# Performance work log

Hardware: AMD Instinct MI355X
Metric: run time of the kernel (lower is better)

The kernel has to match this reference:

```python
import jax, jax.numpy as jnp
import numpy as np
import math

B, L, D_MODEL, D_K, H = 2, 1024, 1024, 1024, 16
HD = D_K // H  # 64, even
EPS = 1e-5


def setup_inputs() -> dict:
    key = jax.random.key(0)
    ks = jax.random.split(key, 16)
    s = 0.02
    inp = {
        'word_embed': jax.random.normal(ks[0], (B, L, D_MODEL), jnp.float32),
        'speaker_embed': jax.random.normal(ks[1], (B, L, D_MODEL), jnp.float32),
        'mask': jnp.broadcast_to(jnp.tril(jnp.ones((L, L), jnp.int32)), (B, L, L)),
        'qw_w': jax.random.normal(ks[2], (D_K, D_MODEL), jnp.float32) * s,
        'qw_b': jnp.zeros((D_K,), jnp.float32),
        'kw_w': jax.random.normal(ks[3], (D_K, D_MODEL), jnp.float32) * s,
        'kw_b': jnp.zeros((D_K,), jnp.float32),
        'qs_w': jax.random.normal(ks[4], (D_K, D_MODEL), jnp.float32) * s,
        'qs_b': jnp.zeros((D_K,), jnp.float32),
        'ks_w': jax.random.normal(ks[5], (D_K, D_MODEL), jnp.float32) * s,
        'ks_b': jnp.zeros((D_K,), jnp.float32),
        'v_w': jax.random.normal(ks[6], (D_K, D_MODEL), jnp.float32) * s,
        'v_b': jnp.zeros((D_K,), jnp.float32),
        'out_w': jax.random.normal(ks[7], (D_MODEL, D_K), jnp.float32) * s,
        'out_b': jnp.zeros((D_MODEL,), jnp.float32),
        'gamma': jnp.ones((HD,), jnp.float32),
        'beta': jnp.zeros((HD,), jnp.float32),
    }
    return inp


def _rotary_tables(seq_len, dim, dtype):
    pos = jnp.arange(seq_len, dtype=dtype)[:, None]  # [L,1]
    div = jnp.exp(jnp.arange(0, dim, 2, dtype=dtype) * (-math.log(10000.0) / dim))
    return jnp.sin(pos * div), jnp.cos(pos * div)  # each [L, dim//2]


def _rotary(x, sin, cos):
    # x: [B,H,L,HD]; NOTE: original concatenates halves (non-interleaved output)
    x1, x2 = x[..., 0::2], x[..., 1::2]
    return jnp.concatenate([x1 * cos - x2 * sin, x1 * sin + x2 * cos], axis=-1)


def _layernorm(x, gamma, beta):
    mu = jnp.mean(x, axis=-1, keepdims=True)
    var = jnp.mean(jnp.square(x - mu), axis=-1, keepdims=True)
    return (x - mu) * jax.lax.rsqrt(var + EPS) * gamma + beta


def _split(x):
    b, l, _ = x.shape
    return x.reshape(b, l, H, HD).transpose(0, 2, 1, 3)  # [B,H,L,HD]


def reference(word_embed, speaker_embed, mask, qw_w, qw_b, kw_w, kw_b,
              qs_w, qs_b, ks_w, ks_b, v_w, v_b, out_w, out_b, gamma, beta):
    proj = lambda x, w, b: jnp.einsum('bld,kd->blk', x, w) + b
    qw = _split(proj(word_embed, qw_w, qw_b))
    kw = _split(proj(word_embed, kw_w, kw_b))
    qs = _split(proj(speaker_embed, qs_w, qs_b))
    ks = _split(proj(speaker_embed, ks_w, ks_b))
    v = _split(proj(word_embed, v_w, v_b))

    sin, cos = _rotary_tables(word_embed.shape[1], HD, word_embed.dtype)
    ln = lambda x: _layernorm(_rotary(x, sin, cos), gamma, beta)
    qw, kw, qs, ks = ln(qw), ln(kw), ln(qs), ln(ks)

    scores = (jnp.einsum('bhqd,bhkd->bhqk', qw, kw)
              + jnp.einsum('bhqd,bhkd->bhqk', qs, ks)) / math.sqrt(2 * HD)
    scores = jnp.where(mask[:, None] == 0, -jnp.inf, scores)
    attn = jax.nn.softmax(scores, axis=-1)  # dropout is eval-mode no-op
    out = jnp.einsum('bhqk,bhkd->bhqd', attn, v)
    out = out.transpose(0, 2, 1, 3).reshape(out.shape[0], out.shape[2], D_K)
    out = jnp.einsum('blk,dk->bld', out, out_w) + out_b
    return (out, attn)
```

## Files before the change

### kernel.cpp

```cpp
#include <hip/hip_runtime.h>
#include <cstdint>
#include <cstddef>

typedef __bf16 bf16x8 __attribute__((ext_vector_type(8)));
typedef float  f32x4  __attribute__((ext_vector_type(4)));
typedef unsigned short ushort8_t __attribute__((ext_vector_type(8)));

__device__ __forceinline__ unsigned short f2bf(float f){
  unsigned u = __builtin_bit_cast(unsigned, f);
  u += 0x7fffu + ((u >> 16) & 1u);
  return (unsigned short)(u >> 16);
}
__device__ __forceinline__ float bf2f(unsigned short s){
  return __builtin_bit_cast(float, ((unsigned)s) << 16);
}

#define MFMA16(a,b,c) __builtin_amdgcn_mfma_f32_16x16x32_bf16((a),(b),(c),0,0,0)

__device__ __forceinline__ void gload16(const void* g, void* lds){
  __builtin_amdgcn_global_load_lds(
      (const __attribute__((address_space(1))) void*)g,
      (__attribute__((address_space(3))) void*)lds, 16, 0, 0);
}

// ... 25 lines not shown
    float ang = (float)pos * inv;
    float sv, cv; sincosf(ang, &sv, &cv);
    FB[5120 + idx]         = sv;
    FB[5120 + 32768 + idx] = cv;
  } else if (idx < 33792){
    int i = idx - 32768;
    FB[i] = qwb[i]; FB[1024+i] = kwb[i]; FB[2048+i] = vb[i];
    FB[3072+i] = qsb[i]; FB[3072+1024+i] = ksb[i];
  }

  const size_t total = 2621440;
  for (size_t c = (size_t)blockIdx.x*256 + threadIdx.x; c < total;
       c += (size_t)gridDim.x*256){
    const float* src; size_t dst; size_t i;
    if (c < 524288)       { src = word; dst = E_XW; i = c; }
    else if (c < 1048576) { src = spk;  dst = E_XS; i = c - 524288; }
    else {
      size_t t = c - 1048576; int seg = (int)(t >> 18); i = t & 262143;
      switch (seg){
        case 0:  src = qww; dst = E_WWORD;                      break;
        case 1:  src = kww; dst = E_WWORD + (size_t)1048576;    break;
        case 2:  src = vw;  dst = E_WWORD + (size_t)2097152;    break;
        case 3:  src = qsw; dst = E_WSPK;                       break;
        case 4:  src = ksw; dst = E_WSPK  + (size_t)1048576;    break;
        default: src = outw; dst = E_WOUT;                      break;
      }
    }
    float4 v = ((const float4*)src)[i];
    ushort4 o; o.x = f2bf(v.x); o.y = f2bf(v.y); o.z = f2bf(v.z); o.w = f2bf(v.w);
    ((ushort4*)(wsb + dst))[i] = o;
  }
}

template<int NF>
__device__ __forceinline__ void gemm_body(
    const unsigned short* __restrict__ A, const unsigned short* __restrict__ Bw,
    const float* __restrict__ bias, void* __restrict__ Cv,
    int N, int K, int bid, int out_bf16,
    unsigned short* As, unsigned short* Bs)
{
  const int BN = NF*32;
  const int nbn = N / BN;
  const int bm = bid / nbn, bn = bid % nbn;
  const int tid = threadIdx.x;
  const int l = tid & 63, w = tid >> 6;
  const int wm = w >> 1, wn = w & 1;
  const int li = l & 15, lg = l >> 4;

  f32x4 acc[4][NF];
  #pragma unroll
  for (int a = 0; a < 4; a++)
    #pragma unroll
    for (int b = 0; b < NF; b++) acc[a][b] = (f32x4){0.f,0.f,0.f,0.f};

  const int colS = (l & 3) * 8;
  const size_t aBase = (size_t)(bm*128) * K;
  const size_t bBase = (size_t)(bn*BN) * K;

  for (int kt = 0; kt < K; kt += 32){
    #pragma unroll
    for (int j = 0; j < 2; j++){
      int row = (w*2 + j)*16 + (l >> 2);
      gload16(A + aBase + (size_t)row*K + kt + colS, &As[(size_t)(w*2+j)*512]);
    }
    if (NF == 4){
      #pragma unroll
      for (int j = 0; j < 2; j++){
        int row = (w*2 + j)*16 + (l >> 2);
        gload16(Bw + bBase + (size_t)row*K + kt + colS, &Bs[(size_t)(w*2+j)*512]);
      }
    } else {
      int row = w*16 + (l >> 2);
      gload16(Bw + bBase + (size_t)row*K + kt + colS, &Bs[(size_t)w*512]);
    }
    asm volatile("s_waitcnt vmcnt(0)" ::: "memory");
    __syncthreads();

    bf16x8 af[4], bfr[NF];
    const int ko = lg * 8;
    #pragma unroll
    for (int fm = 0; fm < 4; fm++)
      af[fm] = *(const bf16x8*)&As[(wm*64 + fm*16 + li)*32 + ko];
    #pragma unroll
    for (int fn = 0; fn < NF; fn++)
      bfr[fn] = *(const bf16x8*)&Bs[(wn*(NF*16) + fn*16 + li)*32 + ko];
    #pragma unroll
    for (int fm = 0; fm < 4; fm++)
      #pragma unroll
      for (int fn = 0; fn < NF; fn++)
        acc[fm][fn] = MFMA16(af[fm], bfr[fn], acc[fm][fn]);
    __syncthreads();
  }

  #pragma unroll
  for (int fm = 0; fm < 4; fm++){
    int m0 = bm*128 + wm*64 + fm*16 + lg*4;
    #pragma unroll
    for (int fn = 0; fn < NF; fn++){
      int n = bn*BN + wn*(NF*16) + fn*16 + li;
      float bv = bias ? bias[n] : 0.f;
      #pragma unroll
      for (int r = 0; r < 4; r++){
        float v = acc[fm][fn][r] + bv;
        if (out_bf16) ((unsigned short*)Cv)[(size_t)(m0+r)*N + n] = f2bf(v);
        else          ((float*)Cv)[(size_t)(m0+r)*N + n] = v;
      }
    }
  }
}

__global__ __launch_bounds__(256) void gemm_qkv(
    const unsigned short* __restrict__ XW, const unsigned short* __restrict__ WWORD,
    const unsigned short* __restrict__ XS, const unsigned short* __restrict__ WSPK,
    const float* __restrict__ FB,
    unsigned short* __restrict__ PWORD, unsigned short* __restrict__ PSPK)
{
  __shared__ unsigned short As[128*32];
  __shared__ unsigned short Bs[128*32];
  int bid = blockIdx.x;
  if (bid < 384)
    gemm_body<4>(XW, WWORD, FB,        PWORD, 3072, 1024, bid,       1, As, Bs);
  else
    gemm_body<4>(XS, WSPK,  FB + 3072, PSPK,  2048, 1024, bid - 384, 1, As, Bs);
}

__global__ __launch_bounds__(256) void gemm_out(
    const unsigned short* __restrict__ CTX, const unsigned short* __restrict__ WOUT,
    const float* __restrict__ outb, float* __restrict__ outp)
{
  __shared__ unsigned short As[128*32];
  __shared__ unsigned short Bs[64*32];
  gemm_body<2>(CTX, WOUT, outb, outp, 1024, 1024, blockIdx.x, 0, As, Bs);
}

__global__ __launch_bounds__(256) void postproc(
    unsigned short* __restrict__ Pw, unsigned short* __restrict__ Ps,
    const float* __restrict__ gamma, const float* __restrict__ beta,
    const float* __restrict__ TS, const float* __restrict__ TC,
    unsigned short* __restrict__ VT)
{
  __shared__ float lds[2320];
  int bx = blockIdx.x;
  int t = threadIdx.x;
  if (bx < 4096){
    int sec = bx & 3, rp = bx >> 2;
    int half = t >> 7, c = t & 127;
    int row = rp*2 + half;
    int seg = c >> 3, j = c & 7;
    unsigned short* p;
    if      (sec == 0) p = Pw + (size_t)row*3072 +        seg*64;
    else if (sec == 1) p = Pw + (size_t)row*3072 + 1024 + seg*64;
    else if (sec == 2) p = Ps + (size_t)row*2048 +        seg*64;
    else               p = Ps + (size_t)row*2048 + 1024 + seg*64;
    int pos = row & 1023;
    int sl  = half*16 + seg;

    ushort8_t xv = *(const ushort8_t*)(p + j*8);
    float4 sv = *(const float4*)&TS[pos*32 + j*4];
    float4 cv = *(const float4*)&TC[pos*32 + j*4];
    float ss[4] = {sv.x, sv.y, sv.z, sv.w};
    float cc[4] = {cv.x, cv.y, cv.z, cv.w};
    float y1[4], y2[4];
    #pragma unroll
    for (int k = 0; k < 4; k++){
      float x0 = bf2f(xv[2*k]), x1 = bf2f(xv[2*k+1]);
      y1[k] = x0*cc[k] - x1*ss[k];
      y2[k] = x0*ss[k] + x1*cc[k];
    }
    *(float4*)&lds[sl*68 + j*4]      = (float4){y1[0], y1[1], y1[2], y1[3]};
    *(float4*)&lds[sl*68 + 32 + j*4] = (float4){y2[0], y2[1], y2[2], y2[3]};
    __syncthreads();

    float4 a0 = *(const float4*)&lds[sl*68 + j*8];
    float4 a1 = *(const float4*)&lds[sl*68 + j*8 + 4];
    float v[8] = {a0.x, a0.y, a0.z, a0.w, a1.x, a1.y, a1.z, a1.w};
    float s = 0.f;
    #pragma unroll
    for (int k = 0; k < 8; k++) s += v[k];
    #pragma unroll
    for (int o = 1; o < 8; o <<= 1) s += __shfl_xor(s, o);
    float mu = s * (1.f/64.f);
    float sq = 0.f;
    #pragma unroll
    for (int k = 0; k < 8; k++){ float d = v[k] - mu; sq += d*d; }
    #pragma unroll
    for (int o = 1; o < 8; o <<= 1) sq += __shfl_xor(sq, o);
    float rs = rsqrtf(sq * (1.f/64.f) + 1e-5f);
    float4 g0 = *(const float4*)&gamma[j*8], g1 = *(const float4*)&gamma[j*8+4];
    float4 b0 = *(const float4*)&beta[j*8],  b1 = *(const float4*)&beta[j*8+4];
    float gg[8] = {g0.x,g0.y,g0.z,g0.w,g1.x,g1.y,g1.z,g1.w};
    float bb[8] = {b0.x,b0.y,b0.z,b0.w,b1.x,b1.y,b1.z,b1.w};
    ushort8_t o8;
    #pragma unroll
    for (int k = 0; k < 8; k++) o8[k] = f2bf((v[k]-mu)*rs*gg[k] + bb[k]);
    *(ushort8_t*)(p + j*8) = o8;
  } else {
    unsigned short* tp = (unsigned short*)lds;
    int bid2 = bx - 4096;
    int bh = bid2 >> 4, lt = bid2 & 15;
    int b = bh >> 4, h = bh & 15;
    #pragma unroll
    for (int i = 0; i < 2; i++){
      int cc2 = t + i*256;
      int row = cc2 >> 3, co = (cc2 & 7)*8;
      const unsigned short* src = Pw + (size_t)(b*1024 + lt*64 + row)*3072 + 2048 + h*64 + co;
      *(uint4*)&tp[row*72 + co] = *(const uint4*)src;
    }
    __syncthreads();
    int d = t >> 2, jb = (t & 3)*16;
    unsigned short o[16];
    #pragma unroll
    for (int j = 0; j < 16; j++) o[j] = tp[(jb + j)*72 + d];
    unsigned short* dst = VT + ((size_t)bh*64 + d)*1024 + lt*64 + jb;
    *(uint4*)dst       = *(uint4*)&o[0];
    *(uint4*)(dst + 8) = *(uint4*)&o[8];
  }
}

__global__ __launch_bounds__(512) void attn_fused(
    const unsigned short* __restrict__ Pw, const unsigned short* __restrict__ Ps,
    const unsigned short* __restrict__ VTg,
    float* __restrict__ attn, unsigned short* __restrict__ Ctx)
{
  __shared__ unsigned short SL[36864];

  int bx = blockIdx.x;
  int b = bx >> 7, rem = bx & 127, h = rem >> 3, qq = rem & 7;
  int maxkt = 15 - qq;
  int tid = threadIdx.x;
  int w = tid >> 6, l = tid & 63;
  int g = w >> 2, wsub = w & 3;
  int qt = g ? maxkt : qq;
  int lg = l >> 4, li = l & 15;
  int q0 = qt*64 + wsub*16;
  int bh = b*16 + h;

  int srow = tid >> 3, scb = tid & 7;
  const unsigned short* gKW = Pw + (size_t)(b*1024)*3072 + 1024 + h*64;
  const unsigned short* gKS = Ps + (size_t)(b*1024)*2048 + 1024 + h*64;
  const unsigned short* gVT = VTg + (size_t)bh*64*1024;
  unsigned short* pt = SL + 27648 + w*1152;

  bf16x8 aqw[2], aqs[2];
  {
    int q = q0 + li;
    const unsigned short* pqw = Pw + (size_t)(b*1024 + q)*3072 + h*64 + lg*8;
    const unsigned short* pqs = Ps + (size_t)(b*1024 + q)*2048 + h*64 + lg*8;
    aqw[0] = *(const bf16x8*)pqw;  aqw[1] = *(const bf16x8*)(pqw + 32);
    aqs[0] = *(const bf16x8*)pqs;  aqs[1] = *(const bf16x8*)(pqs + 32);
  }
  const float rscale = 0.08838834764831845f;

  uint4 rkw, rks, rvt;

  float ps4[4] = {0.f, 0.f, 0.f, 0.f};
  rkw = *(const uint4*)(gKW + (size_t)srow*3072 + scb*8);
  rks = *(const uint4*)(gKS + (size_t)srow*2048 + scb*8);
  *(uint4*)(SL +        srow*72 + scb*8) = rkw;
  *(uint4*)(SL + 9216 + srow*72 + scb*8) = rks;

  for (int kt = 0; kt <= maxkt; ++kt){
    int buf = kt & 1;
    if (kt < maxkt){
      rkw = *(const uint4*)(gKW + (size_t)((kt+1)*64 + srow)*3072 + scb*8);
      rks = *(const uint4*)(gKS + (size_t)((kt+1)*64 + srow)*2048 + scb*8);
    }
    __syncthreads();
    if (kt <= qt){
      const unsigned short* KWt = SL +        buf*4608;
      const unsigned short* KSt = SL + 9216 + buf*4608;
      f32x4 s[4];
      #pragma unroll
      for (int fn = 0; fn < 4; fn++){
        s[fn] = (f32x4){0.f,0.f,0.f,0.f};
        int rr = (fn*16 + li)*72;
        bf16x8 k0 = *(const bf16x8*)(KWt + rr + lg*8);
        bf16x8 k1 = *(const bf16x8*)(KWt + rr + 32 + lg*8);
        bf16x8 k2 = *(const bf16x8*)(KSt + rr + lg*8);
        bf16x8 k3 = *(const bf16x8*)(KSt + rr + 32 + lg*8);
        s[fn] = MFMA16(aqw[0], k0, s[fn]);
        s[fn] = MFMA16(aqw[1], k1, s[fn]);
        s[fn] = MFMA16(aqs[0], k2, s[fn]);
        s[fn] = MFMA16(aqs[1], k3, s[fn]);
      }
      #pragma unroll
      for (int r = 0; r < 4; r++){
        int q = q0 + lg*4 + r;
        #pragma unroll
        for (int fn = 0; fn < 4; fn++){
          int k = kt*64 + fn*16 + li;
          float e = __expf(s[fn][r] * rscale);
          ps4[r] += (k <= q) ? e : 0.f;
        }
      }
    }
    if (kt < maxkt){
      int nb = buf ^ 1;
      *(uint4*)(SL +        nb*4608 + srow*72 + scb*8) = rkw;
      *(uint4*)(SL + 9216 + nb*4608 + srow*72 + scb*8) = rks;
    }
  }
  #pragma unroll
  for (int r = 0; r < 4; r++){
    #pragma unroll
    for (int o = 1; o < 16; o <<= 1) ps4[r] += __shfl_xor(ps4[r], o);
  }
  float rinv[4];
  #pragma unroll
  for (int r = 0; r < 4; r++) rinv[r] = 1.f / ps4[r];

  __syncthreads();
  rkw = *(const uint4*)(gKW + (size_t)srow*3072 + scb*8);
  rks = *(const uint4*)(gKS + (size_t)srow*2048 + scb*8);
  rvt = *(const uint4*)(gVT + (size_t)srow*1024 + scb*8);
  *(uint4*)(SL +         srow*72 + scb*8) = rkw;
  *(uint4*)(SL +  9216 + srow*72 + scb*8) = rks;
  *(uint4*)(SL + 18432 + srow*72 + scb*8) = rvt;

  f32x4 c[4];
  #pragma unroll
  for (int fn = 0; fn < 4; fn++) c[fn] = (f32x4){0.f,0.f,0.f,0.f};

  for (int kt = 0; kt < 16; ++kt){
    int buf = kt & 1;
    if (kt < maxkt){
      rkw = *(const uint4*)(gKW + (size_t)((kt+1)*64 + srow)*3072 + scb*8);
      rks = *(const uint4*)(gKS + (size_t)((kt+1)*64 + srow)*2048 + scb*8);
      rvt = *(const uint4*)(gVT + (size_t)srow*1024 + (kt+1)*64 + scb*8);
    }
    __syncthreads();
    float* abase = attn + ((size_t)bh*1024 + q0 + li)*1024 + kt*64;
    if (kt <= qt){
      const unsigned short* KWt = SL +         buf*4608;
      const unsigned short* KSt = SL +  9216 + buf*4608;
      const unsigned short* VTt = SL + 18432 + buf*4608;
      f32x4 s[4];
      #pragma unroll
      for (int fn = 0; fn < 4; fn++){
        s[fn] = (f32x4){0.f,0.f,0.f,0.f};
        int rr = (fn*16 + li)*72;
        bf16x8 k0 = *(const bf16x8*)(KWt + rr + lg*8);
        bf16x8 k1 = *(const bf16x8*)(KWt + rr + 32 + lg*8);
        bf16x8 k2 = *(const bf16x8*)(KSt + rr + lg*8);
        bf16x8 k3 = *(const bf16x8*)(KSt + rr + 32 + lg*8);
        s[fn] = MFMA16(aqw[0], k0, s[fn]);
        s[fn] = MFMA16(aqw[1], k1, s[fn]);
        s[fn] = MFMA16(aqs[0], k2, s[fn]);
        s[fn] = MFMA16(aqs[1], k3, s[fn]);
      }
      #pragma unroll
      for (int fn = 0; fn < 4; fn++){
        #pragma unroll
        for (int r = 0; r < 4; r++){
          int k = kt*64 + fn*16 + li;
          int q = q0 + lg*4 + r;
          float pp = (k <= q) ? __expf(s[fn][r] * rscale) * rinv[r] : 0.f;
          pt[(lg*4 + r)*72 + fn*16 + li] = f2bf(pp);
        }
      }
      asm volatile("s_waitcnt lgkmcnt(0)" ::: "memory");
      __builtin_amdgcn_sched_barrier(0);
      bf16x8 af0 = *(const bf16x8*)(pt + li*72 + lg*8);
      bf16x8 af1 = *(const bf16x8*)(pt + li*72 + 32 + lg*8);
      ushort8_t u0 = __builtin_bit_cast(ushort8_t, af0);
      ushort8_t u1 = __builtin_bit_cast(ushort8_t, af1);
      *(float4*)(abase + lg*8)          = (float4){bf2f(u0[0]),bf2f(u0[1]),bf2f(u0[2]),bf2f(u0[3])};
      *(float4*)(abase + lg*8 + 4)      = (float4){bf2f(u0[4]),bf2f(u0[5]),bf2f(u0[6]),bf2f(u0[7])};
      *(float4*)(abase + 32 + lg*8)     = (float4){bf2f(u1[0]),bf2f(u1[1]),bf2f(u1[2]),bf2f(u1[3])};
      *(float4*)(abase + 32 + lg*8 + 4) = (float4){bf2f(u1[4]),bf2f(u1[5]),bf2f(u1[6]),bf2f(u1[7])};
      #pragma unroll
      for (int fn = 0; fn < 4; fn++){
        int rr = (fn*16 + li)*72;
        bf16x8 v0 = *(const bf16x8*)(VTt + rr + lg*8);
        bf16x8 v1 = *(const bf16x8*)(VTt + rr + 32 + lg*8);
        c[fn] = MFMA16(af0, v0, c[fn]);
        c[fn] = MFMA16(af1, v1, c[fn]);
      }
    } else {
      float4 z = {0.f, 0.f, 0.f, 0.f};
      *(float4*)(abase + lg*8)          = z;
      *(float4*)(abase + lg*8 + 4)      = z;
      *(float4*)(abase + 32 + lg*8)     = z;
      *(float4*)(abase + 32 + lg*8 + 4) = z;
    }
    if (kt < maxkt){
      int nb = buf ^ 1;
      *(uint4*)(SL +         nb*4608 + srow*72 + scb*8) = rkw;
      *(uint4*)(SL +  9216 + nb*4608 + srow*72 + scb*8) = rks;
      *(uint4*)(SL + 18432 + nb*4608 + srow*72 + scb*8) = rvt;
    }
  }

  #pragma unroll
  for (int fn = 0; fn < 4; fn++){
    #pragma unroll
    for (int r = 0; r < 4; r++){
      int q = q0 + lg*4 + r;
      int d = fn*16 + li;
      Ctx[(size_t)(b*1024 + q)*1024 + h*64 + d] = f2bf(c[fn][r]);
    }
  }
}

extern "C" void kernel_launch(void* const* d_in, const int* in_sizes, int n_in,
                              void* d_out, int out_size, void* d_ws, size_t ws_size,
                              hipStream_t stream)
{
  (void)in_sizes; (void)n_in; (void)out_size; (void)ws_size;
  const float* word = (const float*)d_in[0];
  const float* spk  = (const float*)d_in[1];
  const float* qww  = (const float*)d_in[3];
  const float* qwb  = (const float*)d_in[4];
  const float* kww  = (const float*)d_in[5];
  const float* kwb  = (const float*)d_in[6];
  const float* qsw  = (const float*)d_in[7];
  const float* qsb  = (const float*)d_in[8];
  const float* ksw  = (const float*)d_in[9];
  const float* ksb  = (const float*)d_in[10];
  const float* vw   = (const float*)d_in[11];
  const float* vb   = (const float*)d_in[12];
  const float* outw = (const float*)d_in[13];
  const float* outb = (const float*)d_in[14];
  const float* gamma= (const float*)d_in[15];
  const float* beta = (const float*)d_in[16];

  unsigned short* U = (unsigned short*)d_ws;
  unsigned short* XW    = U + E_XW;
  unsigned short* XS    = U + E_XS;
  unsigned short* WWORD = U + E_WWORD;
  unsigned short* WSPK  = U + E_WSPK;
  unsigned short* WOUT  = U + E_WOUT;
  unsigned short* PWORD = U + E_PWORD;
  unsigned short* PSPK  = U + E_PSPK;
  unsigned short* VT    = U + E_VT;
  unsigned short* CTX   = U + E_CTX;
  float* FB = (float*)(U + E_END);
  float* TS = FB + 5120;
  float* TC = TS + 32768;

  float* outp = (float*)d_out;
  float* attn = outp + (size_t)2*1024*1024;

  convert_all<<<4096, 256, 0, stream>>>(word, spk, qww, kww, vw, qsw, ksw, outw,
                                        qwb, kwb, vb, qsb, ksb, U, FB);
  gemm_qkv<<<640, 256, 0, stream>>>(XW, WWORD, XS, WSPK, FB, PWORD, PSPK);
  postproc<<<4608, 256, 0, stream>>>(PWORD, PSPK, gamma, beta, TS, TC, VT);
  attn_fused<<<256, 512, 0, stream>>>(PWORD, PSPK, VT, attn, CTX);
  gemm_out<<<256, 256, 0, stream>>>(CTX, WOUT, outb, outp);
}
```

Measured before the change: 120.9 us.

## Fuse rotary+layernorm and V transpose into QKV GEMM epilogue; resplit attention blocks

The postproc kernel is removed. Rotary embedding, layernorm and the V transpose now run in the QKV GEMM epilogue through a per-wave LDS tile, writing a 2048-wide normalized projection buffer and the transposed V directly. This drops a full read-write pass over the projections and one kernel launch. The attention kernel changes from 512-thread blocks that pair short and long query tiles to 256-thread blocks with one query tile each, scheduled longest first. It also adds s_setprio around the MFMA loops and moves the zero-fill of the masked region into a separate tail loop. Risks include a one-pass variance formula with less numerical stability, and load imbalance now handled only by block ordering.

```diff
diff --git a/kernel.cpp b/kernel.cpp
--- a/kernel.cpp
+++ b/kernel.cpp
@@ -81,96 +81,176 @@
   }
 }
 
-template<int NF>
-__device__ __forceinline__ void gemm_body(
-    const unsigned short* __restrict__ A, const unsigned short* __restrict__ Bw,
-    const float* __restrict__ bias, void* __restrict__ Cv,
-    int N, int K, int bid, int out_bf16,
-    unsigned short* As, unsigned short* Bs)
+__global__ __launch_bounds__(256) void gemm_qkv(
+    const unsigned short* __restrict__ XW, const unsigned short* __restrict__ WWORD,
+    const unsigned short* __restrict__ XS, const unsigned short* __restrict__ WSPK,
+    const float* __restrict__ FB, const float* __restrict__ TS, const float* __restrict__ TC,
+    const float* __restrict__ gamma, const float* __restrict__ beta,
+    unsigned short* __restrict__ PWORD, unsigned short* __restrict__ PSPK,
+    unsigned short* __restrict__ VT)
 {
-  const int BN = NF*32;
-  const int nbn = N / BN;
+  __shared__ unsigned short As[128*32];
+  __shared__ unsigned short Bs[128*32];
+  __shared__ unsigned short TILE[4][64*72];
+
+  int bid = blockIdx.x;
+  const unsigned short *A, *Bw;
+  const float* bias;
+  int N, isspk;
+  if (bid < 384){ A = XW; Bw = WWORD; bias = FB;        N = 3072; isspk = 0; }
+  else          { bid -= 384; A = XS; Bw = WSPK; bias = FB + 3072; N = 2048; isspk = 1; }
+
+  const int K = 1024;
+  const int nbn = N >> 7;
   const int bm = bid / nbn, bn = bid % nbn;
   const int tid = threadIdx.x;
   const int l = tid & 63, w = tid >> 6;
   const int wm = w >> 1, wn = w & 1;
   const int li = l & 15, lg = l >> 4;
 
-  f32x4 acc[4][NF];
+  f32x4 acc[4][4];
   #pragma unroll
   for (int a = 0; a < 4; a++)
     #pragma unroll
-    for (int b = 0; b < NF; b++) acc[a][b] = (f32x4){0.f,0.f,0.f,0.f};
+    for (int b2 = 0; b2 < 4; b2++) acc[a][b2] = (f32x4){0.f,0.f,0.f,0.f};
 
   const int colS = (l & 3) * 8;
   const size_t aBase = (size_t)(bm*128) * K;
-  const size_t bBase = (size_t)(bn*BN) * K;
+  const size_t bBase = (size_t)(bn*128) * K;
 
   for (int kt = 0; kt < K; kt += 32){
     #pragma unroll
     for (int j = 0; j < 2; j++){
       int row = (w*2 + j)*16 + (l >> 2);
-      gload16(A + aBase + (size_t)row*K + kt + colS, &As[(size_t)(w*2+j)*512]);
-    }
-    if (NF == 4){
-      #pragma unroll
-      for (int j = 0; j < 2; j++){
-        int row = (w*2 + j)*16 + (l >> 2);
-        gload16(Bw + bBase + (size_t)row*K + kt + colS, &Bs[(size_t)(w*2+j)*512]);
-      }
-    } else {
-      int row = w*16 + (l >> 2);
-      gload16(Bw + bBase + (size_t)row*K + kt + colS, &Bs[(size_t)w*512]);
+      gload16(A  + aBase + (size_t)row*K + kt + colS, &As[(size_t)(w*2+j)*512]);
+      gload16(Bw + bBase + (size_t)row*K + kt + colS, &Bs[(size_t)(w*2+j)*512]);
     }
     asm volatile("s_waitcnt vmcnt(0)" ::: "memory");
     __syncthreads();
 
-    bf16x8 af[4], bfr[NF];
+    bf16x8 af[4], bfr[4];
     const int ko = lg * 8;
     #pragma unroll
     for (int fm = 0; fm < 4; fm++)
       af[fm] = *(const bf16x8*)&As[(wm*64 + fm*16 + li)*32 + ko];
     #pragma unroll
-    for (int fn = 0; fn < NF; fn++)
-      bfr[fn] = *(const bf16x8*)&Bs[(wn*(NF*16) + fn*16 + li)*32 + ko];
+    for (int fn = 0; fn < 4; fn++)
+      bfr[fn] = *(const bf16x8*)&Bs[(wn*64 + fn*16 + li)*32 + ko];
     #pragma unroll
     for (int fm = 0; fm < 4; fm++)
       #pragma unroll
-      for (int fn = 0; fn < NF; fn++)
+      for (int fn = 0; fn < 4; fn++)
         acc[fm][fn] = MFMA16(af[fm], bfr[fn], acc[fm][fn]);
     __syncthreads();
   }
 
-  #pragma unroll
-  for (int fm = 0; fm < 4; fm++){
-    int m0 = bm*128 + wm*64 + fm*16 + lg*4;
-    #pragma unroll
-    for (int fn = 0; fn < NF; fn++){
-      int n = bn*BN + wn*(NF*16) + fn*16 + li;
-      float bv = bias ? bias[n] : 0.f;
-      #pragma unroll
-      for (int r = 0; r < 4; r++){
-        float v = acc[fm][fn][r] + bv;
-        if (out_bf16) ((unsigned short*)Cv)[(size_t)(m0+r)*N + n] = f2bf(v);
-        else          ((float*)Cv)[(size_t)(m0+r)*N + n] = v;
-      }
-    }
-  }
-}
-
-__global__ __launch_bounds__(256) void gemm_qkv(
-    const unsigned short* __restrict__ XW, const unsigned short* __restrict__ WWORD,
-    const unsigned short* __restrict__ XS, const unsigned short* __restrict__ WSPK,
-    const float* __restrict__ FB,
-    unsigned short* __restrict__ PWORD, unsigned short* __restrict__ PSPK)
-{
-  __shared__ unsigned short As[128*32];
-  __shared__ unsigned short Bs[128*32];
-  int bid = blockIdx.x;
-  if (bid < 384)
-    gemm_body<4>(XW, WWORD, FB,        PWORD, 3072, 1024, bid,       1, As, Bs);
-  else
-    gemm_body<4>(XS, WSPK,  FB + 3072, PSPK,  2048, 1024, bid - 384, 1, As, Bs);
+  const int n0 = bn*128 + wn*64;
+  const int m0 = bm*128 + wm*64;
+  unsigned short* tile = TILE[w];
+
+  float bv[4];
+  #pragma unroll
+  for (int fn = 0; fn < 4; fn++) bv[fn] = bias[n0 + fn*16 + li];
+  #pragma unroll
+  for (int fm = 0; fm < 4; fm++)
+    #pragma unroll
+    for (int fn = 0; fn < 4; fn++)
+      #pragma unroll
+      for (int r = 0; r < 4; r++)
+        tile[(fm*16 + lg*4 + r)*72 + fn*16 + li] = f2bf(acc[fm][fn][r] + bv[fn]);
+  asm volatile("s_waitcnt lgkmcnt(0)" ::: "memory");
+
+  const int lane = l;
+  if (!isspk && n0 >= 2048){
+    int h  = (n0 - 2048) >> 6;
+    int bb = m0 >> 10, l0 = m0 & 1023;
+    unsigned short* dst = VT + ((size_t)(bb*16 + h)*64 + lane)*1024 + l0;
+    #pragma unroll
+    for (int g2 = 0; g2 < 8; ++g2){
+      unsigned short tmp[8];
+      #pragma unroll
+      for (int t2 = 0; t2 < 8; ++t2) tmp[t2] = tile[(g2*8 + t2)*72 + lane];
+      *(uint4*)(dst + g2*8) = *(uint4*)tmp;
+    }
+  } else {
+    int pos = (m0 + lane) & 1023;
+    float vsum = 0.f, vsq = 0.f;
+    #pragma unroll
+    for (int t2 = 0; t2 < 4; ++t2){
+      ushort8_t xa = *(ushort8_t*)&tile[lane*72 + t2*16];
+      ushort8_t xb = *(ushort8_t*)&tile[lane*72 + t2*16 + 8];
+      float4 s0 = *(const float4*)&TS[pos*32 + t2*8];
+      float4 s1 = *(const float4*)&TS[pos*32 + t2*8 + 4];
+      float4 c0 = *(const float4*)&TC[pos*32 + t2*8];
+      float4 c1 = *(const float4*)&TC[pos*32 + t2*8 + 4];
+      float sa[8] = {s0.x,s0.y,s0.z,s0.w,s1.x,s1.y,s1.z,s1.w};
+      float ca[8] = {c0.x,c0.y,c0.z,c0.w,c1.x,c1.y,c1.z,c1.w};
+      #pragma unroll
+      for (int u = 0; u < 8; ++u){
+        unsigned short e0 = (u < 4) ? xa[2*u]     : xb[2*u - 8];
+        unsigned short e1 = (u < 4) ? xa[2*u + 1] : xb[2*u - 7];
+        float xe = bf2f(e0), xo = bf2f(e1);
+        float ya = xe*ca[u] - xo*sa[u];
+        float yb = xe*sa[u] + xo*ca[u];
+        vsum += ya + yb;
+        vsq  += ya*ya + yb*yb;
+      }
+    }
+    float mu  = vsum * (1.f/64.f);
+    float var = vsq * (1.f/64.f) - mu*mu;
+    float rs  = rsqrtf(var + 1e-5f);
+    ushort8_t oz[8];
+    #pragma unroll
+    for (int t2 = 0; t2 < 4; ++t2){
+      ushort8_t xa = *(ushort8_t*)&tile[lane*72 + t2*16];
+      ushort8_t xb = *(ushort8_t*)&tile[lane*72 + t2*16 + 8];
+      float4 s0 = *(const float4*)&TS[pos*32 + t2*8];
+      float4 s1 = *(const float4*)&TS[pos*32 + t2*8 + 4];
+      float4 c0 = *(const float4*)&TC[pos*32 + t2*8];
+      float4 c1 = *(const float4*)&TC[pos*32 + t2*8 + 4];
+      float4 ga0 = *(const float4*)&gamma[t2*8];
+      float4 ga1 = *(const float4*)&gamma[t2*8 + 4];
+      float4 gb0 = *(const float4*)&gamma[32 + t2*8];
+      float4 gb1 = *(const float4*)&gamma[32 + t2*8 + 4];
+      float4 bb0 = *(const float4*)&beta[t2*8];
+      float4 bb1 = *(const float4*)&beta[t2*8 + 4];
+      float4 bc0 = *(const float4*)&beta[32 + t2*8];
+      float4 bc1 = *(const float4*)&beta[32 + t2*8 + 4];
+      float sa[8] = {s0.x,s0.y,s0.z,s0.w,s1.x,s1.y,s1.z,s1.w};
+      float ca[8] = {c0.x,c0.y,c0.z,c0.w,c1.x,c1.y,c1.z,c1.w};
+      float g_a[8] = {ga0.x,ga0.y,ga0.z,ga0.w,ga1.x,ga1.y,ga1.z,ga1.w};
+      float g_b[8] = {gb0.x,gb0.y,gb0.z,gb0.w,gb1.x,gb1.y,gb1.z,gb1.w};
+      float b_a[8] = {bb0.x,bb0.y,bb0.z,bb0.w,bb1.x,bb1.y,bb1.z,bb1.w};
+      float b_b[8] = {bc0.x,bc0.y,bc0.z,bc0.w,bc1.x,bc1.y,bc1.z,bc1.w};
+      ushort8_t za, zb;
+      #pragma unroll
+      for (int u = 0; u < 8; ++u){
+        unsigned short e0 = (u < 4) ? xa[2*u]     : xb[2*u - 8];
+        unsigned short e1 = (u < 4) ? xa[2*u + 1] : xb[2*u - 7];
+        float xe = bf2f(e0), xo = bf2f(e1);
+        float ya = xe*ca[u] - xo*sa[u];
+        float yb = xe*sa[u] + xo*ca[u];
+        za[u] = f2bf((ya - mu)*rs*g_a[u] + b_a[u]);
+        zb[u] = f2bf((yb - mu)*rs*g_b[u] + b_b[u]);
+      }
+      oz[2*t2]     = za;
+      oz[2*t2 + 1] = zb;
+    }
+    #pragma unroll
+    for (int t2 = 0; t2 < 4; ++t2){
+      *(ushort8_t*)&tile[lane*72 + t2*8]      = oz[2*t2];
+      *(ushort8_t*)&tile[lane*72 + 32 + t2*8] = oz[2*t2 + 1];
+    }
+    asm volatile("s_waitcnt lgkmcnt(0)" ::: "memory");
+    unsigned short* P = isspk ? PSPK : PWORD;
+    int rr2 = lane >> 3, cc2 = lane & 7;
+    #pragma unroll
+    for (int g2 = 0; g2 < 8; ++g2){
+      int row = g2*8 + rr2;
+      uint4 vv = *(uint4*)&tile[row*72 + cc2*8];
+      *(uint4*)(P + (size_t)(m0 + row)*2048 + n0 + cc2*8) = vv;
+    }
+  }
 }
 
 __global__ __launch_bounds__(256) void gemm_out(
@@ -179,113 +259,83 @@
 {
   __shared__ unsigned short As[128*32];
   __shared__ unsigned short Bs[64*32];
-  gemm_body<2>(CTX, WOUT, outb, outp, 1024, 1024, blockIdx.x, 0, As, Bs);
-}
-
-__global__ __launch_bounds__(256) void postproc(
-    unsigned short* __restrict__ Pw, unsigned short* __restrict__ Ps,
-    const float* __restrict__ gamma, const float* __restrict__ beta,
-    const float* __restrict__ TS, const float* __restrict__ TC,
-    unsigned short* __restrict__ VT)
-{
-  __shared__ float lds[2320];
-  int bx = blockIdx.x;
-  int t = threadIdx.x;
-  if (bx < 4096){
-    int sec = bx & 3, rp = bx >> 2;
-    int half = t >> 7, c = t & 127;
-    int row = rp*2 + half;
-    int seg = c >> 3, j = c & 7;
-    unsigned short* p;
-    if      (sec == 0) p = Pw + (size_t)row*3072 +        seg*64;
-    else if (sec == 1) p = Pw + (size_t)row*3072 + 1024 + seg*64;
-    else if (sec == 2) p = Ps + (size_t)row*2048 +        seg*64;
-    else               p = Ps + (size_t)row*2048 + 1024 + seg*64;
-    int pos = row & 1023;
-    int sl  = half*16 + seg;
-
-    ushort8_t xv = *(const ushort8_t*)(p + j*8);
-    float4 sv = *(const float4*)&TS[pos*32 + j*4];
-    float4 cv = *(const float4*)&TC[pos*32 + j*4];
-    float ss[4] = {sv.x, sv.y, sv.z, sv.w};
-    float cc[4] = {cv.x, cv.y, cv.z, cv.w};
-    float y1[4], y2[4];
-    #pragma unroll
-    for (int k = 0; k < 4; k++){
-      float x0 = bf2f(xv[2*k]), x1 = bf2f(xv[2*k+1]);
-      y1[k] = x0*cc[k] - x1*ss[k];
-      y2[k] = x0*ss[k] + x1*cc[k];
-    }
-    *(float4*)&lds[sl*68 + j*4]      = (float4){y1[0], y1[1], y1[2], y1[3]};
-    *(float4*)&lds[sl*68 + 32 + j*4] = (float4){y2[0], y2[1], y2[2], y2[3]};
+  const int N = 1024, K = 1024;
+  const int nbn = N >> 6;
+  const int bm = blockIdx.x / nbn, bn = blockIdx.x % nbn;
+  const int tid = threadIdx.x;
+  const int l = tid & 63, w = tid >> 6;
+  const int wm = w >> 1, wn = w & 1;
+  const int li = l & 15, lg = l >> 4;
+
+  f32x4 acc[4][2];
+  #pragma unroll
+  for (int a = 0; a < 4; a++){ acc[a][0] = (f32x4){0,0,0,0}; acc[a][1] = (f32x4){0,0,0,0}; }
+
+  const int colS = (l & 3) * 8;
+  const size_t aBase = (size_t)(bm*128) * K;
+  const size_t bBase = (size_t)(bn*64) * K;
+
+  for (int kt = 0; kt < K; kt += 32){
+    #pragma unroll
+    for (int j = 0; j < 2; j++){
+      int row = (w*2 + j)*16 + (l >> 2);
+      gload16(CTX + aBase + (size_t)row*K + kt + colS, &As[(size_t)(w*2+j)*512]);
+    }
+    {
+      int row = w*16 + (l >> 2);
+      gload16(WOUT + bBase + (size_t)row*K + kt + colS, &Bs[(size_t)w*512]);
+    }
+    asm volatile("s_waitcnt vmcnt(0)" ::: "memory");
     __syncthreads();
 
-    float4 a0 = *(const float4*)&lds[sl*68 + j*8];
-    float4 a1 = *(const float4*)&lds[sl*68 + j*8 + 4];
-    float v[8] = {a0.x, a0.y, a0.z, a0.w, a1.x, a1.y, a1.z, a1.w};
-    float s = 0.f;
-    #pragma unroll
-    for (int k = 0; k < 8; k++) s += v[k];
-    #pragma unroll
-    for (int o = 1; o < 8; o <<= 1) s += __shfl_xor(s, o);
-    float mu = s * (1.f/64.f);
-    float sq = 0.f;
-    #pragma unroll
-    for (int k = 0; k < 8; k++){ float d = v[k] - mu; sq += d*d; }
-    #pragma unroll
-    for (int o = 1; o < 8; o <<= 1) sq += __shfl_xor(sq, o);
-    float rs = rsqrtf(sq * (1.f/64.f) + 1e-5f);
-    float4 g0 = *(const float4*)&gamma[j*8], g1 = *(const float4*)&gamma[j*8+4];
-    float4 b0 = *(const float4*)&beta[j*8],  b1 = *(const float4*)&beta[j*8+4];
-    float gg[8] = {g0.x,g0.y,g0.z,g0.w,g1.x,g1.y,g1.z,g1.w};
-    float bb[8] = {b0.x,b0.y,b0.z,b0.w,b1.x,b1.y,b1.z,b1.w};
-    ushort8_t o8;
-    #pragma unroll
-    for (int k = 0; k < 8; k++) o8[k] = f2bf((v[k]-mu)*rs*gg[k] + bb[k]);
-    *(ushort8_t*)(p + j*8) = o8;
-  } else {
-    unsigned short* tp = (unsigned short*)lds;
-    int bid2 = bx - 4096;
-    int bh = bid2 >> 4, lt = bid2 & 15;
-    int b = bh >> 4, h = bh & 15;
-    #pragma unroll
-    for (int i = 0; i < 2; i++){
-      int cc2 = t + i*256;
-      int row = cc2 >> 3, co = (cc2 & 7)*8;
-      const unsigned short* src = Pw + (size_t)(b*1024 + lt*64 + row)*3072 + 2048 + h*64 + co;
-      *(uint4*)&tp[row*72 + co] = *(const uint4*)src;
-    }
+    bf16x8 af[4], bfr[2];
+    const int ko = lg * 8;
+    #pragma unroll
+    for (int fm = 0; fm < 4; fm++)
+      af[fm] = *(const bf16x8*)&As[(wm*64 + fm*16 + li)*32 + ko];
+    #pragma unroll
+    for (int fn = 0; fn < 2; fn++)
+      bfr[fn] = *(const bf16x8*)&Bs[(wn*32 + fn*16 + li)*32 + ko];
+    #pragma unroll
+    for (int fm = 0; fm < 4; fm++)
+      #pragma unroll
+      for (int fn = 0; fn < 2; fn++)
+        acc[fm][fn] = MFMA16(af[fm], bfr[fn], acc[fm][fn]);
     __syncthreads();
-    int d = t >> 2, jb = (t & 3)*16;
-    unsigned short o[16];
-    #pragma unroll
-    for (int j = 0; j < 16; j++) o[j] = tp[(jb + j)*72 + d];
-    unsigned short* dst = VT + ((size_t)bh*64 + d)*1024 + lt*64 + jb;
-    *(uint4*)dst       = *(uint4*)&o[0];
-    *(uint4*)(dst + 8) = *(uint4*)&o[8];
-  }
-}
-
-__global__ __launch_bounds__(512) void attn_fused(
+  }
+
+  #pragma unroll
+  for (int fm = 0; fm < 4; fm++){
+    int mr0 = bm*128 + wm*64 + fm*16 + lg*4;
+    #pragma unroll
+    for (int fn = 0; fn < 2; fn++){
+      int n = bn*64 + wn*32 + fn*16 + li;
+      float bvv = outb[n];
+      #pragma unroll
+      for (int r = 0; r < 4; r++)
+        outp[(size_t)(mr0 + r)*N + n] = acc[fm][fn][r] + bvv;
+    }
+  }
+}
+
+__global__ __launch_bounds__(256) void attn_fused(
     const unsigned short* __restrict__ Pw, const unsigned short* __restrict__ Ps,
     const unsigned short* __restrict__ VTg,
     float* __restrict__ attn, unsigned short* __restrict__ Ctx)
 {
-  __shared__ unsigned short SL[36864];
+  __shared__ unsigned short SL[32256];
 
   int bx = blockIdx.x;
-  int b = bx >> 7, rem = bx & 127, h = rem >> 3, qq = rem & 7;
-  int maxkt = 15 - qq;
+  int b = bx >> 8, rem = bx & 255, h = rem >> 4;
+  int qt = 15 - (rem & 15);
   int tid = threadIdx.x;
   int w = tid >> 6, l = tid & 63;
-  int g = w >> 2, wsub = w & 3;
-  int qt = g ? maxkt : qq;
   int lg = l >> 4, li = l & 15;
-  int q0 = qt*64 + wsub*16;
+  int q0 = qt*64 + w*16;
   int bh = b*16 + h;
 
-  int srow = tid >> 3, scb = tid & 7;
-  const unsigned short* gKW = Pw + (size_t)(b*1024)*3072 + 1024 + h*64;
+  int sr = tid >> 3, sc = tid & 7;
+  const unsigned short* gKW = Pw + (size_t)(b*1024)*2048 + 1024 + h*64;
   const unsigned short* gKS = Ps + (size_t)(b*1024)*2048 + 1024 + h*64;
   const unsigned short* gVT = VTg + (size_t)bh*64*1024;
   unsigned short* pt = SL + 27648 + w*1152;
@@ -293,32 +343,39 @@
   bf16x8 aqw[2], aqs[2];
   {
     int q = q0 + li;
-    const unsigned short* pqw = Pw + (size_t)(b*1024 + q)*3072 + h*64 + lg*8;
+    const unsigned short* pqw = Pw + (size_t)(b*1024 + q)*2048 + h*64 + lg*8;
     const unsigned short* pqs = Ps + (size_t)(b*1024 + q)*2048 + h*64 + lg*8;
     aqw[0] = *(const bf16x8*)pqw;  aqw[1] = *(const bf16x8*)(pqw + 32);
     aqs[0] = *(const bf16x8*)pqs;  aqs[1] = *(const bf16x8*)(pqs + 32);
   }
   const float rscale = 0.08838834764831845f;
 
-  uint4 rkw, rks, rvt;
+  uint4 ka0, ka1, kb0, kb1, va0, va1;
 
   float ps4[4] = {0.f, 0.f, 0.f, 0.f};
-  rkw = *(const uint4*)(gKW + (size_t)srow*3072 + scb*8);
-  rks = *(const uint4*)(gKS + (size_t)srow*2048 + scb*8);
-  *(uint4*)(SL +        srow*72 + scb*8) = rkw;
-  *(uint4*)(SL + 9216 + srow*72 + scb*8) = rks;
-
-  for (int kt = 0; kt <= maxkt; ++kt){
+  ka0 = *(const uint4*)(gKW + (size_t)sr*2048 + sc*8);
+  ka1 = *(const uint4*)(gKW + (size_t)(sr+32)*2048 + sc*8);
+  kb0 = *(const uint4*)(gKS + (size_t)sr*2048 + sc*8);
+  kb1 = *(const uint4*)(gKS + (size_t)(sr+32)*2048 + sc*8);
+  *(uint4*)(SL + sr*72 + sc*8) = ka0;
+  *(uint4*)(SL + (sr+32)*72 + sc*8) = ka1;
+  *(uint4*)(SL + 9216 + sr*72 + sc*8) = kb0;
+  *(uint4*)(SL + 9216 + (sr+32)*72 + sc*8) = kb1;
+
+  for (int kt = 0; kt <= qt; ++kt){
     int buf = kt & 1;
-    if (kt < maxkt){
-      rkw = *(const uint4*)(gKW + (size_t)((kt+1)*64 + srow)*3072 + scb*8);
-      rks = *(const uint4*)(gKS + (size_t)((kt+1)*64 + srow)*2048 + scb*8);
+    if (kt < qt){
+      ka0 = *(const uint4*)(gKW + (size_t)((kt+1)*64 + sr)*2048 + sc*8);
+      ka1 = *(const uint4*)(gKW + (size_t)((kt+1)*64 + sr+32)*2048 + sc*8);
+      kb0 = *(const uint4*)(gKS + (size_t)((kt+1)*64 + sr)*2048 + sc*8);
+      kb1 = *(const uint4*)(gKS + (size_t)((kt+1)*64 + sr+32)*2048 + sc*8);
     }
     __syncthreads();
-    if (kt <= qt){
-      const unsigned short* KWt = SL +        buf*4608;
+    {
+      const unsigned short* KWt = SL + buf*4608;
       const unsigned short* KSt = SL + 9216 + buf*4608;
       f32x4 s[4];
+      __builtin_amdgcn_s_setprio(1);
       #pragma unroll
       for (int fn = 0; fn < 4; fn++){
         s[fn] = (f32x4){0.f,0.f,0.f,0.f};
@@ -332,6 +389,7 @@
         s[fn] = MFMA16(aqs[0], k2, s[fn]);
         s[fn] = MFMA16(aqs[1], k3, s[fn]);
       }
+      __builtin_amdgcn_s_setprio(0);
       #pragma unroll
       for (int r = 0; r < 4; r++){
         int q = q0 + lg*4 + r;
@@ -343,10 +401,12 @@
         }
       }
     }
-    if (kt < maxkt){
+    if (kt < qt){
       int nb = buf ^ 1;
-      *(uint4*)(SL +        nb*4608 + srow*72 + scb*8) = rkw;
-      *(uint4*)(SL + 9216 + nb*4608 + srow*72 + scb*8) = rks;
+      *(uint4*)(SL + nb*4608 + sr*72 + sc*8) = ka0;
+      *(uint4*)(SL + nb*4608 + (sr+32)*72 + sc*8) = ka1;
+      *(uint4*)(SL + 9216 + nb*4608 + sr*72 + sc*8) = kb0;
+      *(uint4*)(SL + 9216 + nb*4608 + (sr+32)*72 + sc*8) = kb1;
     }
   }
   #pragma unroll
@@ -359,31 +419,41 @@
   for (int r = 0; r < 4; r++) rinv[r] = 1.f / ps4[r];
 
   __syncthreads();
-  rkw = *(const uint4*)(gKW + (size_t)srow*3072 + scb*8);
-  rks = *(const uint4*)(gKS + (size_t)srow*2048 + scb*8);
-  rvt = *(const uint4*)(gVT + (size_t)srow*1024 + scb*8);
-  *(uint4*)(SL +         srow*72 + scb*8) = rkw;
-  *(uint4*)(SL +  9216 + srow*72 + scb*8) = rks;
-  *(uint4*)(SL + 18432 + srow*72 + scb*8) = rvt;
+  ka0 = *(const uint4*)(gKW + (size_t)sr*2048 + sc*8);
+  ka1 = *(const uint4*)(gKW + (size_t)(sr+32)*2048 + sc*8);
+  kb0 = *(const uint4*)(gKS + (size_t)sr*2048 + sc*8);
+  kb1 = *(const uint4*)(gKS + (size_t)(sr+32)*2048 + sc*8);
+  va0 = *(const uint4*)(gVT + (size_t)sr*1024 + sc*8);
+  va1 = *(const uint4*)(gVT + (size_t)(sr+32)*1024 + sc*8);
+  *(uint4*)(SL + sr*72 + sc*8) = ka0;
+  *(uint4*)(SL + (sr+32)*72 + sc*8) = ka1;
+  *(uint4*)(SL + 9216 + sr*72 + sc*8) = kb0;
+  *(uint4*)(SL + 9216 + (sr+32)*72 + sc*8) = kb1;
+  *(uint4*)(SL + 18432 + sr*72 + sc*8) = va0;
+  *(uint4*)(SL + 18432 + (sr+32)*72 + sc*8) = va1;
 
   f32x4 c[4];
   #pragma unroll
   for (int fn = 0; fn < 4; fn++) c[fn] = (f32x4){0.f,0.f,0.f,0.f};
 
-  for (int kt = 0; kt < 16; ++kt){
+  for (int kt = 0; kt <= qt; ++kt){
     int buf = kt & 1;
-    if (kt < maxkt){
-      rkw = *(const uint4*)(gKW + (size_t)((kt+1)*64 + srow)*3072 + scb*8);
-      rks = *(const uint4*)(gKS + (size_t)((kt+1)*64 + srow)*2048 + scb*8);
-      rvt = *(const uint4*)(gVT + (size_t)srow*1024 + (kt+1)*64 + scb*8);
+    if (kt < qt){
+      ka0 = *(const uint4*)(gKW + (size_t)((kt+1)*64 + sr)*2048 + sc*8);
+      ka1 = *(const uint4*)(gKW + (size_t)((kt+1)*64 + sr+32)*2048 + sc*8);
+      kb0 = *(const uint4*)(gKS + (size_t)((kt+1)*64 + sr)*2048 + sc*8);
+      kb1 = *(const uint4*)(gKS + (size_t)((kt+1)*64 + sr+32)*2048 + sc*8);
+      va0 = *(const uint4*)(gVT + (size_t)sr*1024 + (kt+1)*64 + sc*8);
+      va1 = *(const uint4*)(gVT + (size_t)(sr+32)*1024 + (kt+1)*64 + sc*8);
     }
     __syncthreads();
     float* abase = attn + ((size_t)bh*1024 + q0 + li)*1024 + kt*64;
-    if (kt <= qt){
-      const unsigned short* KWt = SL +         buf*4608;
-      const unsigned short* KSt = SL +  9216 + buf*4608;
+    {
+      const unsigned short* KWt = SL + buf*4608;
+      const unsigned short* KSt = SL + 9216 + buf*4608;
       const unsigned short* VTt = SL + 18432 + buf*4608;
       f32x4 s[4];
+      __builtin_amdgcn_s_setprio(1);
       #pragma unroll
       for (int fn = 0; fn < 4; fn++){
         s[fn] = (f32x4){0.f,0.f,0.f,0.f};
@@ -397,6 +467,7 @@
         s[fn] = MFMA16(aqs[0], k2, s[fn]);
         s[fn] = MFMA16(aqs[1], k3, s[fn]);
       }
+      __builtin_amdgcn_s_setprio(0);
       #pragma unroll
       for (int fn = 0; fn < 4; fn++){
         #pragma unroll
@@ -417,6 +488,7 @@
       *(float4*)(abase + lg*8 + 4)      = (float4){bf2f(u0[4]),bf2f(u0[5]),bf2f(u0[6]),bf2f(u0[7])};
       *(float4*)(abase + 32 + lg*8)     = (float4){bf2f(u1[0]),bf2f(u1[1]),bf2f(u1[2]),bf2f(u1[3])};
       *(float4*)(abase + 32 + lg*8 + 4) = (float4){bf2f(u1[4]),bf2f(u1[5]),bf2f(u1[6]),bf2f(u1[7])};
+      __builtin_amdgcn_s_setprio(1);
       #pragma unroll
       for (int fn = 0; fn < 4; fn++){
         int rr = (fn*16 + li)*72;
@@ -425,19 +497,26 @@
         c[fn] = MFMA16(af0, v0, c[fn]);
         c[fn] = MFMA16(af1, v1, c[fn]);
       }
-    } else {
-      float4 z = {0.f, 0.f, 0.f, 0.f};
-      *(float4*)(abase + lg*8)          = z;
-      *(float4*)(abase + lg*8 + 4)      = z;
-      *(float4*)(abase + 32 + lg*8)     = z;
-      *(float4*)(abase + 32 + lg*8 + 4) = z;
-    }
-    if (kt < maxkt){
+      __builtin_amdgcn_s_setprio(0);
+    }
+    if (kt < qt){
       int nb = buf ^ 1;
-      *(uint4*)(SL +         nb*4608 + srow*72 + scb*8) = rkw;
-      *(uint4*)(SL +  9216 + nb*4608 + srow*72 + scb*8) = rks;
-      *(uint4*)(SL + 18432 + nb*4608 + srow*72 + scb*8) = rvt;
-    }
+      *(uint4*)(SL + nb*4608 + sr*72 + sc*8) = ka0;
+      *(uint4*)(SL + nb*4608 + (sr+32)*72 + sc*8) = ka1;
+      *(uint4*)(SL + 9216 + nb*4608 + sr*72 + sc*8) = kb0;
+      *(uint4*)(SL + 9216 + nb*4608 + (sr+32)*72 + sc*8) = kb1;
+      *(uint4*)(SL + 18432 + nb*4608 + sr*72 + sc*8) = va0;
+      *(uint4*)(SL + 18432 + nb*4608 + (sr+32)*72 + sc*8) = va1;
+    }
+  }
+
+  for (int kt = qt + 1; kt < 16; ++kt){
+    float* abase = attn + ((size_t)bh*1024 + q0 + li)*1024 + kt*64;
+    float4 z = {0.f, 0.f, 0.f, 0.f};
+    *(float4*)(abase + lg*8)          = z;
+    *(float4*)(abase + lg*8 + 4)      = z;
+    *(float4*)(abase + 32 + lg*8)     = z;
+    *(float4*)(abase + 32 + lg*8 + 4) = z;
   }
 
   #pragma unroll
@@ -492,8 +571,8 @@
 
   convert_all<<<4096, 256, 0, stream>>>(word, spk, qww, kww, vw, qsw, ksw, outw,
                                         qwb, kwb, vb, qsb, ksb, U, FB);
-  gemm_qkv<<<640, 256, 0, stream>>>(XW, WWORD, XS, WSPK, FB, PWORD, PSPK);
-  postproc<<<4608, 256, 0, stream>>>(PWORD, PSPK, gamma, beta, TS, TC, VT);
-  attn_fused<<<256, 512, 0, stream>>>(PWORD, PSPK, VT, attn, CTX);
+  gemm_qkv<<<640, 256, 0, stream>>>(XW, WWORD, XS, WSPK, FB, TS, TC, gamma, beta,
+                                    PWORD, PSPK, VT);
+  attn_fused<<<512, 256, 0, stream>>>(PWORD, PSPK, VT, attn, CTX);
   gemm_out<<<256, 256, 0, stream>>>(CTX, WOUT, outb, outp);
 }
```

Result: slower. 166.1 us (+37.4%).

## Retile QKV and output GEMMs and raise wave priority around MFMA blocks

Applied to the files above, without the earlier changes.

The word-projection GEMM now uses 128x192 tiles (NF=6), so the QKV launch drops from 640 to 512 blocks. The output GEMM becomes a dedicated 64x64-tile kernel launched with 512 blocks instead of 256, which gives more parallelism on a small GEMM. s_setprio is raised around MFMA bursts in the GEMMs and the attention kernel to favour matrix issue over the other waves. Larger QKV tiles add register pressure, and the smaller output tiles reload more operand data from memory.

```diff
diff --git a/kernel.cpp b/kernel.cpp
--- a/kernel.cpp
+++ b/kernel.cpp
@@ -84,10 +84,10 @@
 template<int NF>
 __device__ __forceinline__ void gemm_body(
     const unsigned short* __restrict__ A, const unsigned short* __restrict__ Bw,
-    const float* __restrict__ bias, void* __restrict__ Cv,
-    int N, int K, int bid, int out_bf16,
-    unsigned short* As, unsigned short* Bs)
-{
+    const float* __restrict__ bias, unsigned short* __restrict__ C,
+    int N, int bid, unsigned short* As, unsigned short* Bs)
+{
+  const int K = 1024;
   const int BN = NF*32;
   const int nbn = N / BN;
   const int bm = bid / nbn, bn = bid % nbn;
@@ -102,25 +102,19 @@
     #pragma unroll
     for (int b = 0; b < NF; b++) acc[a][b] = (f32x4){0.f,0.f,0.f,0.f};
 
-  const int colS = (l & 3) * 8;
   const size_t aBase = (size_t)(bm*128) * K;
   const size_t bBase = (size_t)(bn*BN) * K;
 
   for (int kt = 0; kt < K; kt += 32){
     #pragma unroll
     for (int j = 0; j < 2; j++){
-      int row = (w*2 + j)*16 + (l >> 2);
-      gload16(A + aBase + (size_t)row*K + kt + colS, &As[(size_t)(w*2+j)*512]);
-    }
-    if (NF == 4){
-      #pragma unroll
-      for (int j = 0; j < 2; j++){
-        int row = (w*2 + j)*16 + (l >> 2);
-        gload16(Bw + bBase + (size_t)row*K + kt + colS, &Bs[(size_t)(w*2+j)*512]);
-      }
-    } else {
-      int row = w*16 + (l >> 2);
-      gload16(Bw + bBase + (size_t)row*K + kt + colS, &Bs[(size_t)w*512]);
+      int c = (w*2 + j)*64 + l;
+      gload16(A + aBase + (size_t)(c >> 2)*K + kt + (c & 3)*8, &As[(size_t)(w*2+j)*512]);
+    }
+    #pragma unroll
+    for (int j = 0; j < NF/2; j++){
+      int c = (w*(NF/2) + j)*64 + l;
+      gload16(Bw + bBase + (size_t)(c >> 2)*K + kt + (c & 3)*8, &Bs[(size_t)(w*(NF/2)+j)*512]);
     }
     asm volatile("s_waitcnt vmcnt(0)" ::: "memory");
     __syncthreads();
@@ -133,11 +127,13 @@
     #pragma unroll
     for (int fn = 0; fn < NF; fn++)
       bfr[fn] = *(const bf16x8*)&Bs[(wn*(NF*16) + fn*16 + li)*32 + ko];
+    __builtin_amdgcn_s_setprio(1);
     #pragma unroll
     for (int fm = 0; fm < 4; fm++)
       #pragma unroll
       for (int fn = 0; fn < NF; fn++)
         acc[fm][fn] = MFMA16(af[fm], bfr[fn], acc[fm][fn]);
+    __builtin_amdgcn_s_setprio(0);
     __syncthreads();
   }
 
@@ -147,13 +143,10 @@
     #pragma unroll
     for (int fn = 0; fn < NF; fn++){
       int n = bn*BN + wn*(NF*16) + fn*16 + li;
-      float bv = bias ? bias[n] : 0.f;
-      #pragma unroll
-      for (int r = 0; r < 4; r++){
-        float v = acc[fm][fn][r] + bv;
-        if (out_bf16) ((unsigned short*)Cv)[(size_t)(m0+r)*N + n] = f2bf(v);
-        else          ((float*)Cv)[(size_t)(m0+r)*N + n] = v;
-      }
+      float bv = bias[n];
+      #pragma unroll
+      for (int r = 0; r < 4; r++)
+        C[(size_t)(m0+r)*N + n] = f2bf(acc[fm][fn][r] + bv);
     }
   }
 }
@@ -165,21 +158,73 @@
     unsigned short* __restrict__ PWORD, unsigned short* __restrict__ PSPK)
 {
   __shared__ unsigned short As[128*32];
-  __shared__ unsigned short Bs[128*32];
+  __shared__ unsigned short Bs[192*32];
   int bid = blockIdx.x;
-  if (bid < 384)
-    gemm_body<4>(XW, WWORD, FB,        PWORD, 3072, 1024, bid,       1, As, Bs);
+  if (bid < 256)
+    gemm_body<6>(XW, WWORD, FB,        PWORD, 3072, bid,       As, Bs);
   else
-    gemm_body<4>(XS, WSPK,  FB + 3072, PSPK,  2048, 1024, bid - 384, 1, As, Bs);
+    gemm_body<4>(XS, WSPK,  FB + 3072, PSPK,  2048, bid - 256, As, Bs);
 }
 
 __global__ __launch_bounds__(256) void gemm_out(
     const unsigned short* __restrict__ CTX, const unsigned short* __restrict__ WOUT,
     const float* __restrict__ outb, float* __restrict__ outp)
 {
-  __shared__ unsigned short As[128*32];
+  __shared__ unsigned short As[64*32];
   __shared__ unsigned short Bs[64*32];
-  gemm_body<2>(CTX, WOUT, outb, outp, 1024, 1024, blockIdx.x, 0, As, Bs);
+  const int N = 1024, K = 1024;
+  const int bm = blockIdx.x >> 4, bn = blockIdx.x & 15;
+  const int tid = threadIdx.x;
+  const int l = tid & 63, w = tid >> 6;
+  const int wm = w >> 1, wn = w & 1;
+  const int li = l & 15, lg = l >> 4;
+
+  f32x4 acc[2][2];
+  acc[0][0] = (f32x4){0,0,0,0}; acc[0][1] = (f32x4){0,0,0,0};
+  acc[1][0] = (f32x4){0,0,0,0}; acc[1][1] = (f32x4){0,0,0,0};
+
+  const size_t aBase = (size_t)(bm*64) * K;
+  const size_t bBase = (size_t)(bn*64) * K;
+
+  for (int kt = 0; kt < K; kt += 32){
+    {
+      int c = w*64 + l;
+      gload16(CTX  + aBase + (size_t)(c >> 2)*K + kt + (c & 3)*8, &As[(size_t)w*512]);
+      gload16(WOUT + bBase + (size_t)(c >> 2)*K + kt + (c & 3)*8, &Bs[(size_t)w*512]);
+    }
+    asm volatile("s_waitcnt vmcnt(0)" ::: "memory");
+    __syncthreads();
+
+    bf16x8 af[2], bfr[2];
+    const int ko = lg * 8;
+    #pragma unroll
+    for (int fm = 0; fm < 2; fm++)
+      af[fm] = *(const bf16x8*)&As[(wm*32 + fm*16 + li)*32 + ko];
+    #pragma unroll
+    for (int fn = 0; fn < 2; fn++)
+      bfr[fn] = *(const bf16x8*)&Bs[(wn*32 + fn*16 + li)*32 + ko];
+    __builtin_amdgcn_s_setprio(1);
+    #pragma unroll
+    for (int fm = 0; fm < 2; fm++)
+      #pragma unroll
+      for (int fn = 0; fn < 2; fn++)
+        acc[fm][fn] = MFMA16(af[fm], bfr[fn], acc[fm][fn]);
+    __builtin_amdgcn_s_setprio(0);
+    __syncthreads();
+  }
+
+  #pragma unroll
+  for (int fm = 0; fm < 2; fm++){
+    int m0 = bm*64 + wm*32 + fm*16 + lg*4;
+    #pragma unroll
+    for (int fn = 0; fn < 2; fn++){
+      int n = bn*64 + wn*32 + fn*16 + li;
+      float bv = outb[n];
+      #pragma unroll
+      for (int r = 0; r < 4; r++)
+        outp[(size_t)(m0 + r)*N + n] = acc[fm][fn][r] + bv;
+    }
+  }
 }
 
 __global__ __launch_bounds__(256) void postproc(
@@ -319,6 +364,7 @@
       const unsigned short* KWt = SL +        buf*4608;
       const unsigned short* KSt = SL + 9216 + buf*4608;
       f32x4 s[4];
+      __builtin_amdgcn_s_setprio(1);
       #pragma unroll
       for (int fn = 0; fn < 4; fn++){
         s[fn] = (f32x4){0.f,0.f,0.f,0.f};
@@ -332,6 +378,7 @@
         s[fn] = MFMA16(aqs[0], k2, s[fn]);
         s[fn] = MFMA16(aqs[1], k3, s[fn]);
       }
+      __builtin_amdgcn_s_setprio(0);
       #pragma unroll
       for (int r = 0; r < 4; r++){
         int q = q0 + lg*4 + r;
@@ -384,6 +431,7 @@
       const unsigned short* KSt = SL +  9216 + buf*4608;
       const unsigned short* VTt = SL + 18432 + buf*4608;
       f32x4 s[4];
+      __builtin_amdgcn_s_setprio(1);
       #pragma unroll
       for (int fn = 0; fn < 4; fn++){
         s[fn] = (f32x4){0.f,0.f,0.f,0.f};
@@ -397,6 +445,7 @@
         s[fn] = MFMA16(aqs[0], k2, s[fn]);
         s[fn] = MFMA16(aqs[1], k3, s[fn]);
       }
+      __builtin_amdgcn_s_setprio(0);
       #pragma unroll
       for (int fn = 0; fn < 4; fn++){
         #pragma unroll
@@ -417,6 +466,7 @@
       *(float4*)(abase + lg*8 + 4)      = (float4){bf2f(u0[4]),bf2f(u0[5]),bf2f(u0[6]),bf2f(u0[7])};
       *(float4*)(abase + 32 + lg*8)     = (float4){bf2f(u1[0]),bf2f(u1[1]),bf2f(u1[2]),bf2f(u1[3])};
       *(float4*)(abase + 32 + lg*8 + 4) = (float4){bf2f(u1[4]),bf2f(u1[5]),bf2f(u1[6]),bf2f(u1[7])};
+      __builtin_amdgcn_s_setprio(1);
       #pragma unroll
       for (int fn = 0; fn < 4; fn++){
         int rr = (fn*16 + li)*72;
@@ -425,6 +475,7 @@
         c[fn] = MFMA16(af0, v0, c[fn]);
         c[fn] = MFMA16(af1, v1, c[fn]);
       }
+      __builtin_amdgcn_s_setprio(0);
     } else {
       float4 z = {0.f, 0.f, 0.f, 0.f};
       *(float4*)(abase + lg*8)          = z;
@@ -492,8 +543,8 @@
 
   convert_all<<<4096, 256, 0, stream>>>(word, spk, qww, kww, vw, qsw, ksw, outw,
                                         qwb, kwb, vb, qsb, ksb, U, FB);
-  gemm_qkv<<<640, 256, 0, stream>>>(XW, WWORD, XS, WSPK, FB, PWORD, PSPK);
+  gemm_qkv<<<512, 256, 0, stream>>>(XW, WWORD, XS, WSPK, FB, PWORD, PSPK);
   postproc<<<4608, 256, 0, stream>>>(PWORD, PSPK, gamma, beta, TS, TC, VT);
   attn_fused<<<256, 512, 0, stream>>>(PWORD, PSPK, VT, attn, CTX);
-  gemm_out<<<256, 256, 0, stream>>>(CTX, WOUT, outb, outp);
-}
+  gemm_out<<<512, 256, 0, stream>>>(CTX, WOUT, outb, outp);
+}
```

Result: slower. 124.7 us (+3.2%).
